# Kernel tuning notes

Hardware: AMD Instinct MI355X
Metric: run time of the kernel (lower is better)

## Reference

```python
import jax, jax.numpy as jnp
import numpy as np

LN_EPS = 1e-5  # standard LayerNorm eps
OPM_EPS = 1e-3  # module's eps for the mean denominator


def layer_norm(x, g, b):
    mu = jnp.mean(x, axis=-1, keepdims=True)
    var = jnp.mean((x - mu) ** 2, axis=-1, keepdims=True)
    return (x - mu) * jax.lax.rsqrt(var + LN_EPS) * g + b


def setup_inputs() -> dict:
    key = jax.random.key(0)
    ks = jax.random.split(key, 6)
    N, L1, K, L2 = 1, 256, 128, 1024
    c_s, c_m, c_z, ch = 384, 256, 128, 32
    return {
        "s": jax.random.normal(ks[0], (N, L1, c_s), jnp.float32),
        "m": jax.random.normal(ks[1], (N, K, L2, c_m), jnp.float32),
        "ln_ab_g": jnp.ones((c_s,), jnp.float32),
        "ln_ab_b": jnp.zeros((c_s,), jnp.float32),
        "ln_ag_g": jnp.ones((c_m,), jnp.float32),
        "ln_ag_b": jnp.zeros((c_m,), jnp.float32),
        "W_ab": jax.random.normal(ks[2], (c_s, ch), jnp.float32) * 0.02,
        "b_ab": jnp.zeros((ch,), jnp.float32),
        "W_ag": jax.random.normal(ks[3], (c_m, ch), jnp.float32) * 0.02,
        "b_ag": jnp.zeros((ch,), jnp.float32),
        "W_out": jax.random.normal(ks[4], (ch * ch, c_z), jnp.float32) * 0.02,
        "b_out": jnp.zeros((c_z,), jnp.float32),
    }


def reference(s, m, ln_ab_g, ln_ab_b, ln_ag_g, ln_ag_b,
              W_ab, b_ab, W_ag, b_ag, W_out, b_out):
    # s: [N, L1, c_s], m: [N, K, L2, c_m]
    K = m.shape[1]
    ch = W_ab.shape[-1]
    c_z = W_out.shape[-1]

    a = layer_norm(s, ln_ab_g, ln_ab_b) @ W_ab + b_ab          # [N, L1, ch]
    mm = layer_norm(m, ln_ag_g, ln_ag_b) @ W_ag + b_ag          # [N, K, L2, ch]

    # In the original, `a` is repeated along K before the einsum, so it is
    # K-invariant and sum_k a[i,c] * m[k,j,e] == a[i,c] * (sum_k m[k,j,e]).
    m_sum = jnp.sum(mm, axis=1)                                  # [N, L2, ch]

    # outer[n,i,j,c,e] -> flatten (c,e) with c outer -> linear_out
    Wo = W_out.reshape(ch, ch, c_z)                              # [c, e, z]
    z = jnp.einsum('nic,nje,cez->nijz', a, m_sum, Wo) + b_out    # [N, L1, L2, c_z]

    # norm = sum over K of ones == K, plus eps
    return z / (jnp.float32(K) + OPM_EPS)
```

## Files before the change

### kernel.cpp

```cpp
#include <hip/hip_runtime.h>

#define L1V 256
#define L2V 1024
#define KV  128
#define CSV 384
#define CMV 256
#define CHV 32
#define CZV 128

__device__ __forceinline__ float4 f4zero() { return make_float4(0.f,0.f,0.f,0.f); }

__device__ __forceinline__ void ln_accum(const float4 x, float4& xs) {
  float s1 = x.x + x.y + x.z + x.w;
  float s2 = fmaf(x.x, x.x, fmaf(x.y, x.y, fmaf(x.z, x.z, x.w * x.w)));
  #pragma unroll
  for (int off = 32; off > 0; off >>= 1) {
    s1 += __shfl_xor(s1, off, 64);
    s2 += __shfl_xor(s2, off, 64);
  }
  const float mu   = s1 * (1.0f / CMV);
  const float rstd = rsqrtf(s2 * (1.0f / CMV) - mu * mu + 1e-5f);
  xs.x = fmaf(x.x - mu, rstd, xs.x);
  xs.y = fmaf(x.y - mu, rstd, xs.y);
  xs.z = fmaf(x.z - mu, rstd, xs.z);
  xs.w = fmaf(x.w - mu, rstd, xs.w);
}

__global__ __launch_bounds__(256) void msum_kernel(
    const float* __restrict__ m, const float* __restrict__ g,
    const float* __restrict__ b, const float* __restrict__ Wag,
    const float* __restrict__ bag, float* __restrict__ msum)
{
  const int j    = blockIdx.x;
  const int tid  = threadIdx.x;
  const int wave = tid >> 6;
  const int lane = tid & 63;

  const float4* base = (const float4*)m;

  float4 xs = f4zero();
  float4 x0 = base[(((size_t)wave << 10) + j) * 64 + lane];
  float4 x1 = base[(((size_t)(wave + 4) << 10) + j) * 64 + lane];

  for (int k = wave; k < KV; k += 8) {
    float4 n0 = f4zero(), n1 = f4zero();
    if (k + 8  < KV) n0 = base[(((size_t)(k + 8)  << 10) + j) * 64 + lane];
    if (k + 12 < KV) n1 = base[(((size_t)(k + 12) << 10) + j) * 64 + lane];
    ln_accum(x0, xs);
    ln_accum(x1, xs);
    x0 = n0; x1 = n1;
  }

  __shared__ float xsum[4][CMV];
  ((float4*)xsum[wave])[lane] = xs;
  __syncthreads();

  __shared__ float y[CMV];
  y[tid] = (xsum[0][tid] + xsum[1][tid] + xsum[2][tid] + xsum[3][tid]) * g[tid]
           + (float)KV * b[tid];
  __syncthreads();

  const int c     = tid & 31;
  const int chunk = tid >> 5;
  float p = 0.f;
  #pragma unroll
  for (int q = 0; q < 32; ++q) {
    const int e = (chunk << 5) + q;
    p = fmaf(y[e], Wag[(e << 5) + c], p);
  }
  __shared__ float pr[256];
  pr[tid] = p;
  __syncthreads();
  if (tid < 32) {
    float acc = 0.f;
    #pragma unroll
    for (int r = 0; r < 8; ++r) acc += pr[tid + (r << 5)];
    msum[(j << 5) + tid] = acc + (float)KV * bag[tid];
  }
}

__global__ __launch_bounds__(384) void a_kernel(
    const float* __restrict__ s, const float* __restrict__ g,
    const float* __restrict__ b, const float* __restrict__ Wab,
    const float* __restrict__ bab, float* __restrict__ a)
{
  const int i    = blockIdx.x;
  const int tid  = threadIdx.x;
  const int wave = tid >> 6;
  const int lane = tid & 63;

  const float x = s[i * CSV + tid];
  float s1 = x, s2 = x * x;
  #pragma unroll
  for (int off = 32; off > 0; off >>= 1) {
    s1 += __shfl_xor(s1, off, 64);
    s2 += __shfl_xor(s2, off, 64);
  }
  __shared__ float r1[6], r2[6];
  if (lane == 0) { r1[wave] = s1; r2[wave] = s2; }
  __syncthreads();
  float t1 = 0.f, t2 = 0.f;
  #pragma unroll
  for (int w = 0; w < 6; ++w) { t1 += r1[w]; t2 += r2[w]; }
  const float mu   = t1 * (1.0f / CSV);
  const float rstd = rsqrtf(t2 * (1.0f / CSV) - mu * mu + 1e-5f);

  __shared__ float y[CSV];
  y[tid] = (x - mu) * rstd * g[tid] + b[tid];
  __syncthreads();

  const int c     = tid & 31;
  const int chunk = tid >> 5;
  float p = 0.f;
  #pragma unroll
  for (int q = 0; q < 32; ++q) {
    const int e = (chunk << 5) + q;
    p = fmaf(y[e], Wab[(e << 5) + c], p);
  }
  __shared__ float pr[CSV];
  pr[tid] = p;
  __syncthreads();
  if (tid < 32) {
    float acc = 0.f;
    #pragma unroll
    for (int r = 0; r < 12; ++r) acc += pr[tid + (r << 5)];
    a[(i << 5) + tid] = acc + bab[tid];
  }
}

__global__ __launch_bounds__(256) void t_kernel(
    const float* __restrict__ a, const float* __restrict__ Wout,
    float* __restrict__ T)
{
  const int tid = threadIdx.x;
  const int idx = (blockIdx.x << 8) + tid;
  const int i0  = blockIdx.y << 4;

  __shared__ float as[16 * 32];
  #pragma unroll
  for (int r = 0; r < 2; ++r) {
    const int t = (r << 8) + tid;
    as[t] = a[(i0 << 5) + t];
  }
  __syncthreads();

  float w[32];
  #pragma unroll
  for (int c = 0; c < 32; ++c) w[c] = Wout[(c << 12) + idx];

  #pragma unroll 4
  for (int ii = 0; ii < 16; ++ii) {
    float acc = 0.f;
    #pragma unroll
    for (int c = 0; c < 32; ++c)
      acc = fmaf(as[(ii << 5) + c], w[c], acc);
    T[((size_t)(i0 + ii) << 12) + idx] = acc;
  }
}

__global__ __launch_bounds__(256) void out_kernel(
    const float* __restrict__ msum, const float* __restrict__ T,
    const float* __restrict__ bout, float* __restrict__ out)
{
  const int half = blockIdx.x;
  const int i    = blockIdx.y;
  const int tid  = threadIdx.x;
  const int zq   = (tid & 31) << 2;
  const int jg   = tid >> 5;

  float4 Treg[32];
  #pragma unroll
  for (int e = 0; e < 32; ++e)
    Treg[e] = *(const float4*)(T + ((size_t)i << 12) + (e << 7) + zq);

  const float4 bz = *(const float4*)(bout + zq);
  const float inv_norm = 1.0f / ((float)KV + 1e-3f);

  __shared__ float ms[64 * CHV];

  for (int tile = 0; tile < 8; ++tile) {
    const int j0 = (half << 9) + (tile << 6);
    __syncthreads();
    ((float4*)ms)[tid]       = ((const float4*)(msum + ((size_t)j0 << 5)))[tid];
    ((float4*)ms)[tid + 256] = ((const float4*)(msum + ((size_t)j0 << 5)))[tid + 256];
    __syncthreads();

    #pragma unroll
    for (int jj = 0; jj < 8; ++jj) {
      const int j = jg + (jj << 3);
      const float4* mr = (const float4*)(ms + (j << 5));
      float4 acc = f4zero();
      #pragma unroll
      for (int eq = 0; eq < 8; ++eq) {
        const float4 m4 = mr[eq];
        const float4 t0 = Treg[(eq << 2) + 0];
        const float4 t1 = Treg[(eq << 2) + 1];
        const float4 t2 = Treg[(eq << 2) + 2];
        const float4 t3 = Treg[(eq << 2) + 3];
        acc.x = fmaf(m4.x, t0.x, fmaf(m4.y, t1.x, fmaf(m4.z, t2.x, fmaf(m4.w, t3.x, acc.x))));
        acc.y = fmaf(m4.x, t0.y, fmaf(m4.y, t1.y, fmaf(m4.z, t2.y, fmaf(m4.w, t3.y, acc.y))));
        acc.z = fmaf(m4.x, t0.z, fmaf(m4.y, t1.z, fmaf(m4.z, t2.z, fmaf(m4.w, t3.z, acc.z))));
        acc.w = fmaf(m4.x, t0.w, fmaf(m4.y, t1.w, fmaf(m4.z, t2.w, fmaf(m4.w, t3.w, acc.w))));
      }
      float4 o;
      o.x = (acc.x + bz.x) * inv_norm;
      o.y = (acc.y + bz.y) * inv_norm;
      o.z = (acc.z + bz.z) * inv_norm;
      o.w = (acc.w + bz.w) * inv_norm;
      *(float4*)(out + ((size_t)i << 17) + ((size_t)(j0 + j) << 7) + zq) = o;
    }
  }
}

extern "C" void kernel_launch(void* const* d_in, const int* in_sizes, int n_in,
                              void* d_out, int out_size, void* d_ws, size_t ws_size,
                              hipStream_t stream) {
  (void)in_sizes; (void)n_in; (void)out_size; (void)ws_size;
  const float* s    = (const float*)d_in[0];
  const float* m    = (const float*)d_in[1];
  const float* g_ab = (const float*)d_in[2];
  const float* b_ab = (const float*)d_in[3];
  const float* g_ag = (const float*)d_in[4];
  const float* b_ag = (const float*)d_in[5];
  const float* Wab  = (const float*)d_in[6];
  const float* bab  = (const float*)d_in[7];
  const float* Wag  = (const float*)d_in[8];
  const float* bag  = (const float*)d_in[9];
  const float* Wout = (const float*)d_in[10];
  const float* bout = (const float*)d_in[11];
  float* out = (float*)d_out;

  float* msum = (float*)d_ws;
  float* a    = msum + 32768;
  float* T    = a + 8192;

  hipLaunchKernelGGL(msum_kernel, dim3(1024), dim3(256), 0, stream,
                     m, g_ag, b_ag, Wag, bag, msum);
  hipLaunchKernelGGL(a_kernel, dim3(256), dim3(384), 0, stream,
                     s, g_ab, b_ab, Wab, bab, a);
  hipLaunchKernelGGL(t_kernel, dim3(16, 16), dim3(256), 0, stream,
                     a, Wout, T);
  hipLaunchKernelGGL(out_kernel, dim3(2, 256), dim3(256), 0, stream,
                     msum, T, bout, out);
}
```

Before: 280.2 us.

## Fuse msum, a and T kernels into one launch; prefetch msum tiles

```diff
diff --git a/kernel.cpp b/kernel.cpp
--- a/kernel.cpp
+++ b/kernel.cpp
@@ -26,135 +26,139 @@
   xs.w = fmaf(x.w - mu, rstd, xs.w);
 }
 
-__global__ __launch_bounds__(256) void msum_kernel(
-    const float* __restrict__ m, const float* __restrict__ g,
-    const float* __restrict__ b, const float* __restrict__ Wag,
-    const float* __restrict__ bag, float* __restrict__ msum)
+__global__ __launch_bounds__(256) void fused1_kernel(
+    const float* __restrict__ m, const float* __restrict__ g_ag,
+    const float* __restrict__ b_ag, const float* __restrict__ Wag,
+    const float* __restrict__ bag,
+    const float* __restrict__ s, const float* __restrict__ g_ab,
+    const float* __restrict__ b_ab, const float* __restrict__ Wab,
+    const float* __restrict__ bab,
+    const float* __restrict__ Wout,
+    float* __restrict__ msum, float* __restrict__ T)
 {
-  const int j    = blockIdx.x;
-  const int tid  = threadIdx.x;
-  const int wave = tid >> 6;
-  const int lane = tid & 63;
-
-  const float4* base = (const float4*)m;
-
-  float4 xs = f4zero();
-  float4 x0 = base[(((size_t)wave << 10) + j) * 64 + lane];
-  float4 x1 = base[(((size_t)(wave + 4) << 10) + j) * 64 + lane];
-
-  for (int k = wave; k < KV; k += 8) {
-    float4 n0 = f4zero(), n1 = f4zero();
-    if (k + 8  < KV) n0 = base[(((size_t)(k + 8)  << 10) + j) * 64 + lane];
-    if (k + 12 < KV) n1 = base[(((size_t)(k + 12) << 10) + j) * 64 + lane];
-    ln_accum(x0, xs);
-    ln_accum(x1, xs);
-    x0 = n0; x1 = n1;
-  }
-
-  __shared__ float xsum[4][CMV];
-  ((float4*)xsum[wave])[lane] = xs;
-  __syncthreads();
-
-  __shared__ float y[CMV];
-  y[tid] = (xsum[0][tid] + xsum[1][tid] + xsum[2][tid] + xsum[3][tid]) * g[tid]
-           + (float)KV * b[tid];
-  __syncthreads();
-
-  const int c     = tid & 31;
-  const int chunk = tid >> 5;
-  float p = 0.f;
-  #pragma unroll
-  for (int q = 0; q < 32; ++q) {
-    const int e = (chunk << 5) + q;
-    p = fmaf(y[e], Wag[(e << 5) + c], p);
-  }
-  __shared__ float pr[256];
-  pr[tid] = p;
-  __syncthreads();
-  if (tid < 32) {
-    float acc = 0.f;
+  __shared__ float smem[16 * CSV + 16 * CHV];
+  const int tid = threadIdx.x;
+
+  if (blockIdx.x < 1024) {
+    const int j    = blockIdx.x;
+    const int wave = tid >> 6;
+    const int lane = tid & 63;
+
+    const float4* base = (const float4*)m;
+
+    float4 xs = f4zero();
+    float4 x0 = base[(((size_t)wave << 10) + j) * 64 + lane];
+    float4 x1 = base[(((size_t)(wave + 4) << 10) + j) * 64 + lane];
+
+    for (int k = wave; k < KV; k += 8) {
+      float4 n0 = f4zero(), n1 = f4zero();
+      if (k + 8  < KV) n0 = base[(((size_t)(k + 8)  << 10) + j) * 64 + lane];
+      if (k + 12 < KV) n1 = base[(((size_t)(k + 12) << 10) + j) * 64 + lane];
+      ln_accum(x0, xs);
+      ln_accum(x1, xs);
+      x0 = n0; x1 = n1;
+    }
+
+    float* xsum = smem;
+    float* y    = smem + 1024;
+    float* pr   = smem + 1280;
+
+    ((float4*)(xsum + wave * CMV))[lane] = xs;
+    __syncthreads();
+
+    y[tid] = (xsum[tid] + xsum[CMV + tid] + xsum[2 * CMV + tid] + xsum[3 * CMV + tid])
+             * g_ag[tid] + (float)KV * b_ag[tid];
+    __syncthreads();
+
+    const int c     = tid & 31;
+    const int chunk = tid >> 5;
+    float p = 0.f;
     #pragma unroll
-    for (int r = 0; r < 8; ++r) acc += pr[tid + (r << 5)];
-    msum[(j << 5) + tid] = acc + (float)KV * bag[tid];
-  }
-}
-
-__global__ __launch_bounds__(384) void a_kernel(
-    const float* __restrict__ s, const float* __restrict__ g,
-    const float* __restrict__ b, const float* __restrict__ Wab,
-    const float* __restrict__ bab, float* __restrict__ a)
-{
-  const int i    = blockIdx.x;
-  const int tid  = threadIdx.x;
-  const int wave = tid >> 6;
-  const int lane = tid & 63;
-
-  const float x = s[i * CSV + tid];
-  float s1 = x, s2 = x * x;
-  #pragma unroll
-  for (int off = 32; off > 0; off >>= 1) {
-    s1 += __shfl_xor(s1, off, 64);
-    s2 += __shfl_xor(s2, off, 64);
-  }
-  __shared__ float r1[6], r2[6];
-  if (lane == 0) { r1[wave] = s1; r2[wave] = s2; }
-  __syncthreads();
-  float t1 = 0.f, t2 = 0.f;
-  #pragma unroll
-  for (int w = 0; w < 6; ++w) { t1 += r1[w]; t2 += r2[w]; }
-  const float mu   = t1 * (1.0f / CSV);
-  const float rstd = rsqrtf(t2 * (1.0f / CSV) - mu * mu + 1e-5f);
-
-  __shared__ float y[CSV];
-  y[tid] = (x - mu) * rstd * g[tid] + b[tid];
-  __syncthreads();
-
-  const int c     = tid & 31;
-  const int chunk = tid >> 5;
-  float p = 0.f;
-  #pragma unroll
-  for (int q = 0; q < 32; ++q) {
-    const int e = (chunk << 5) + q;
-    p = fmaf(y[e], Wab[(e << 5) + c], p);
-  }
-  __shared__ float pr[CSV];
-  pr[tid] = p;
-  __syncthreads();
-  if (tid < 32) {
-    float acc = 0.f;
+    for (int q = 0; q < 32; ++q) {
+      const int e = (chunk << 5) + q;
+      p = fmaf(y[e], Wag[(e << 5) + c], p);
+    }
+    pr[tid] = p;
+    __syncthreads();
+    if (tid < 32) {
+      float acc = 0.f;
+      #pragma unroll
+      for (int r = 0; r < 8; ++r) acc += pr[tid + (r << 5)];
+      msum[(j << 5) + tid] = acc + (float)KV * bag[tid];
+    }
+  } else {
+    const int bb    = blockIdx.x - 1024;
+    const int chunk = bb & 15;
+    const int i0    = (bb >> 4) << 4;
+    const int idx   = (chunk << 8) + tid;
+
+    float* ys = smem;
+    float* as = smem + 16 * CSV;
+
+    {
+      const int r   = tid >> 4;
+      const int sub = tid & 15;
+      const float4* srow = (const float4*)(s + (size_t)(i0 + r) * CSV);
+      float4 v[6];
+      #pragma unroll
+      for (int q = 0; q < 6; ++q) v[q] = srow[(q << 4) + sub];
+
+      float s1 = 0.f, s2 = 0.f;
+      #pragma unroll
+      for (int q = 0; q < 6; ++q) {
+        s1 += v[q].x + v[q].y + v[q].z + v[q].w;
+        s2 += fmaf(v[q].x, v[q].x, fmaf(v[q].y, v[q].y,
+              fmaf(v[q].z, v[q].z, v[q].w * v[q].w)));
+      }
+      #pragma unroll
+      for (int off = 8; off > 0; off >>= 1) {
+        s1 += __shfl_xor(s1, off, 64);
+        s2 += __shfl_xor(s2, off, 64);
+      }
+      const float mu   = s1 * (1.0f / CSV);
+      const float rstd = rsqrtf(s2 * (1.0f / CSV) - mu * mu + 1e-5f);
+
+      #pragma unroll
+      for (int q = 0; q < 6; ++q) {
+        const float4 gg = ((const float4*)g_ab)[(q << 4) + sub];
+        const float4 bbv = ((const float4*)b_ab)[(q << 4) + sub];
+        float4 yv;
+        yv.x = (v[q].x - mu) * rstd * gg.x + bbv.x;
+        yv.y = (v[q].y - mu) * rstd * gg.y + bbv.y;
+        yv.z = (v[q].z - mu) * rstd * gg.z + bbv.z;
+        yv.w = (v[q].w - mu) * rstd * gg.w + bbv.w;
+        ((float4*)(ys + r * CSV))[(q << 4) + sub] = yv;
+      }
+    }
+    __syncthreads();
+
+    {
+      const int c  = tid & 31;
+      const int r0 = tid >> 5;
+      float acc0 = 0.f, acc1 = 0.f;
+      for (int e = 0; e < CSV; ++e) {
+        const float w = Wab[(e << 5) + c];
+        acc0 = fmaf(ys[r0 * CSV + e], w, acc0);
+        acc1 = fmaf(ys[(r0 + 8) * CSV + e], w, acc1);
+      }
+      const float bc = bab[c];
+      as[(r0 << 5) + c]       = acc0 + bc;
+      as[((r0 + 8) << 5) + c] = acc1 + bc;
+    }
+    __syncthreads();
+
+    float w[32];
     #pragma unroll
-    for (int r = 0; r < 12; ++r) acc += pr[tid + (r << 5)];
-    a[(i << 5) + tid] = acc + bab[tid];
-  }
-}
-
-__global__ __launch_bounds__(256) void t_kernel(
-    const float* __restrict__ a, const float* __restrict__ Wout,
-    float* __restrict__ T)
-{
-  const int tid = threadIdx.x;
-  const int idx = (blockIdx.x << 8) + tid;
-  const int i0  = blockIdx.y << 4;
-
-  __shared__ float as[16 * 32];
-  #pragma unroll
-  for (int r = 0; r < 2; ++r) {
-    const int t = (r << 8) + tid;
-    as[t] = a[(i0 << 5) + t];
-  }
-  __syncthreads();
-
-  float w[32];
-  #pragma unroll
-  for (int c = 0; c < 32; ++c) w[c] = Wout[(c << 12) + idx];
-
-  #pragma unroll 4
-  for (int ii = 0; ii < 16; ++ii) {
-    float acc = 0.f;
-    #pragma unroll
-    for (int c = 0; c < 32; ++c)
-      acc = fmaf(as[(ii << 5) + c], w[c], acc);
-    T[((size_t)(i0 + ii) << 12) + idx] = acc;
+    for (int c = 0; c < 32; ++c) w[c] = Wout[(c << 12) + idx];
+
+    #pragma unroll 4
+    for (int ii = 0; ii < 16; ++ii) {
+      float acc = 0.f;
+      #pragma unroll
+      for (int c = 0; c < 32; ++c)
+        acc = fmaf(as[(ii << 5) + c], w[c], acc);
+      T[((size_t)(i0 + ii) << 12) + idx] = acc;
+    }
   }
 }
 
@@ -176,15 +180,23 @@
   const float4 bz = *(const float4*)(bout + zq);
   const float inv_norm = 1.0f / ((float)KV + 1e-3f);
 
+  const float4* msrc = (const float4*)msum + ((size_t)half << 12);
+  float4 p0 = msrc[tid];
+  float4 p1 = msrc[tid + 256];
+
   __shared__ float ms[64 * CHV];
 
   for (int tile = 0; tile < 8; ++tile) {
+    __syncthreads();
+    ((float4*)ms)[tid]       = p0;
+    ((float4*)ms)[tid + 256] = p1;
+    __syncthreads();
+    if (tile < 7) {
+      p0 = msrc[((tile + 1) << 9) + tid];
+      p1 = msrc[((tile + 1) << 9) + tid + 256];
+    }
+
     const int j0 = (half << 9) + (tile << 6);
-    __syncthreads();
-    ((float4*)ms)[tid]       = ((const float4*)(msum + ((size_t)j0 << 5)))[tid];
-    ((float4*)ms)[tid + 256] = ((const float4*)(msum + ((size_t)j0 << 5)))[tid + 256];
-    __syncthreads();
-
     #pragma unroll
     for (int jj = 0; jj < 8; ++jj) {
       const int j = jg + (jj << 3);
@@ -231,15 +243,12 @@
   float* out = (float*)d_out;
 
   float* msum = (float*)d_ws;
-  float* a    = msum + 32768;
-  float* T    = a + 8192;
-
-  hipLaunchKernelGGL(msum_kernel, dim3(1024), dim3(256), 0, stream,
-                     m, g_ag, b_ag, Wag, bag, msum);
-  hipLaunchKernelGGL(a_kernel, dim3(256), dim3(384), 0, stream,
-                     s, g_ab, b_ab, Wab, bab, a);
-  hipLaunchKernelGGL(t_kernel, dim3(16, 16), dim3(256), 0, stream,
-                     a, Wout, T);
+  float* T    = msum + 32768;
+
+  hipLaunchKernelGGL(fused1_kernel, dim3(1280), dim3(256), 0, stream,
+                     m, g_ag, b_ag, Wag, bag,
+                     s, g_ab, b_ab, Wab, bab,
+                     Wout, msum, T);
   hipLaunchKernelGGL(out_kernel, dim3(2, 256), dim3(256), 0, stream,
                      msum, T, bout, out);
 }
```

Result: no change. 280.5 us (+0.1%).
